# Kernel optimization log

Hardware: AMD Instinct MI355X
Metric: run time of the kernel (lower is better)

The kernel has to match this reference:

```python
import jax, jax.numpy as jnp
import numpy as np

IN_V, OUT_V, IN_E = 64, 64, 64
B, N, E = 2, 1024, 8192


def setup_inputs() -> dict:
    key = jax.random.key(0)
    ks = jax.random.split(key, 8)
    return {
        "H_v": jax.random.normal(ks[0], (B * N, IN_V), dtype=jnp.float32),
        "H_e": jax.random.normal(ks[1], (B * E, IN_E), dtype=jnp.float32),
        "adj_e": jax.random.uniform(ks[2], (B * E, E), dtype=jnp.float32),
        "adj_v": jax.random.uniform(ks[3], (B * N, N), dtype=jnp.float32),
        "T": jax.random.uniform(ks[4], (B * N, E), dtype=jnp.float32),
        "weight": jax.random.normal(ks[5], (IN_V, OUT_V), dtype=jnp.float32) * (1.0 / np.sqrt(OUT_V)),
        "p": jax.random.normal(ks[6], (1, IN_E), dtype=jnp.float32),
        "bias": jax.random.normal(ks[7], (OUT_V,), dtype=jnp.float32) * (1.0 / np.sqrt(OUT_V)),
    }


def reference(H_v, H_e, adj_e, adj_v, T, weight, p, bias):
    # node_layer=True branch of AlternateConvolution
    b = adj_v.shape[0] // adj_v.shape[1]
    n = adj_v.shape[1]
    e = adj_e.shape[1]
    H_v = H_v.reshape(b, n, -1)            # [B,N,in_v]
    H_e = H_e.reshape(b, e, -1)            # [B,E,in_e]
    adj_v = adj_v.reshape(b, n, n)         # [B,N,N]
    T = T.reshape(b, n, e)                 # [B,N,E]
    # diag_embed(H_e @ p^T) then T @ diag @ T^T == row-scale T by (H_e @ p^T) then GEMM
    scale = jnp.einsum('bef,f->be', H_e, p[0])                  # [B,E]
    multiplier1 = jnp.einsum('bne,be,bme->bnm', T, scale, T)    # [B,N,N]
    eye = jnp.eye(n, dtype=bool)
    M1 = jnp.where(eye[None, :, :], jnp.ones_like(multiplier1), multiplier1)
    adjusted_A = M1 * adj_v
    output = jnp.einsum('bnm,bmd->bnd', adjusted_A, H_v @ weight) + bias
    return output, H_e
```

## Files before the change

kernel.cpp:

```cpp
#include <hip/hip_runtime.h>

#define Bb 2
#define Nn 1024
#define Ee 8192
#define DV 64

typedef __attribute__((ext_vector_type(8))) short short8;
typedef __attribute__((ext_vector_type(4))) float floatx4;

static __device__ __forceinline__ unsigned short f2bf(float f) {
    unsigned int u = __float_as_uint(f);
    unsigned int r = (u + 0x7FFFu + ((u >> 16) & 1u)) >> 16;
    return (unsigned short)r;
}

__global__ __launch_bounds__(256) void scale_kernel(const float* __restrict__ He,
                                                    const float* __restrict__ p,
                                                    float* __restrict__ scale) {
    int wave = threadIdx.x >> 6;
    int lane = threadIdx.x & 63;
    int row = blockIdx.x * 4 + wave;
    float v = He[row * 64 + lane] * p[lane];
    #pragma unroll
    for (int off = 32; off > 0; off >>= 1) v += __shfl_xor(v, off);
    if (lane == 0) scale[row] = v;
}

__global__ __launch_bounds__(256) void cast_kernel(const float* __restrict__ T,
                                                   const float* __restrict__ scale,
                                                   unsigned short* __restrict__ Tsc,
                                                   unsigned short* __restrict__ Tpl) {
    size_t i4 = (size_t)blockIdx.x * 256 + threadIdx.x;
    size_t e0 = i4 * 4;
    int b = (int)(e0 >> 23);
    int e = (int)(e0 & 8191);
    floatx4 t = *(const floatx4*)&T[e0];
    floatx4 s = *(const floatx4*)&scale[(size_t)b * Ee + e];
    ushort4 sc, pl;
    sc.x = f2bf(t.x * s.x); sc.y = f2bf(t.y * s.y);
    sc.z = f2bf(t.z * s.z); sc.w = f2bf(t.w * s.w);
    pl.x = f2bf(t.x); pl.y = f2bf(t.y);
    pl.z = f2bf(t.z); pl.w = f2bf(t.w);
    *(ushort4*)&Tsc[e0] = sc;
    *(ushort4*)&Tpl[e0] = pl;
}

__global__ __launch_bounds__(256) void hw_kernel(const float* __restrict__ Hv,
                                                 const float* __restrict__ W,
                                                 float* __restrict__ HWo) {
    __shared__ float Ws[64 * 64];
    __shared__ float Hvs[4 * 64];
    int t = threadIdx.x;
    for (int i = t; i < 4096; i += 256) Ws[i] = W[i];
    int r0 = blockIdx.x * 4;
    Hvs[t] = Hv[(size_t)r0 * 64 + t];
    __syncthreads();
    int d = t & 63, rr = t >> 6;
    float acc = 0.f;
    #pragma unroll
    for (int c = 0; c < 64; ++c) acc += Hvs[rr * 64 + c] * Ws[c * 64 + d];
    HWo[(size_t)(r0 + rr) * 64 + d] = acc;
}

__global__ __launch_bounds__(256, 2) void mm_kernel(const unsigned short* __restrict__ Tsc,
                                                    const unsigned short* __restrict__ Tpl,
                                                    float* __restrict__ Ppart) {
    __shared__ __attribute__((aligned(16))) unsigned short As[128 * 64];
    __shared__ __attribute__((aligned(16))) unsigned short Bs[128 * 64];
    const int t = threadIdx.x;
    const int tile = blockIdx.x;
    const int b = blockIdx.y;
    const int s = blockIdx.z;

    int i = 0, rem = tile;
    while (rem >= 8 - i) { rem -= 8 - i; ++i; }
    const int j = i + rem;
    const int n0 = i * 128, m0 = j * 128;

    const int lane = t & 63;
    const int w = t >> 6;
    const int wr = w >> 1, wc = w & 1;
    const int quad = lane >> 4;
    const int l15 = lane & 15;
    const int l7 = l15 & 7;

    const int lr = lane >> 3;
    const int lc = (lane & 7) ^ lr;

    const int kc0 = (s * 128) / 7 * 64;
    const int kc1 = ((s + 1) * 128) / 7 * 64;

    const unsigned short* gA = Tsc + ((size_t)b * Nn + n0 + w * 32 + lr) * Ee + kc0 + lc * 8;
    const unsigned short* gB = Tpl + ((size_t)b * Nn + m0 + w * 32 + lr) * Ee + kc0 + lc * 8;
    unsigned short* lA = As + (w * 32) * 64 + lane * 8;
    unsigned short* lB = Bs + (w * 32) * 64 + lane * 8;

    floatx4 acc[4][4];
    #pragma unroll
    for (int a = 0; a < 4; ++a)
        #pragma unroll
        for (int c = 0; c < 4; ++c) acc[a][c] = (floatx4){0.f, 0.f, 0.f, 0.f};

    for (int k0 = kc0; k0 < kc1; k0 += 64) {
        #pragma unroll
        for (int u = 0; u < 4; ++u) {
            __builtin_amdgcn_global_load_lds(
                (const __attribute__((address_space(1))) unsigned int*)(gA + (size_t)u * 8 * Ee),
                (__attribute__((address_space(3))) unsigned int*)(lA + u * 8 * 64), 16, 0, 0);
            __builtin_amdgcn_global_load_lds(
                (const __attribute__((address_space(1))) unsigned int*)(gB + (size_t)u * 8 * Ee),
                (__attribute__((address_space(3))) unsigned int*)(lB + u * 8 * 64), 16, 0, 0);
        }
        gA += 64; gB += 64;
        __syncthreads();
        #pragma unroll
        for (int kk8 = 0; kk8 < 8; kk8 += 4) {
            short8 af[4], bf[4];
            #pragma unroll
            for (int a = 0; a < 4; ++a)
                af[a] = *(const short8*)&As[(wr * 64 + a * 16 + l15) * 64 + ((kk8 + quad) ^ l7) * 8];
            #pragma unroll
            for (int c = 0; c < 4; ++c)
                bf[c] = *(const short8*)&Bs[(wc * 64 + c * 16 + l15) * 64 + ((kk8 + quad) ^ l7) * 8];
            #pragma unroll
            for (int a = 0; a < 4; ++a)
                #pragma unroll
                for (int c = 0; c < 4; ++c)
                    acc[a][c] = __builtin_amdgcn_mfma_f32_16x16x32_bf16(af[a], bf[c], acc[a][c], 0, 0, 0);
        }
        __syncthreads();
    }

    float* P = Ppart + (((size_t)(b * 36 + tile)) * 7 + s) * 16384;
    #pragma unroll
    for (int a = 0; a < 4; ++a)
        #pragma unroll
        for (int c = 0; c < 4; ++c)
            #pragma unroll
            for (int v = 0; v < 4; ++v) {
                int r = wr * 64 + a * 16 + quad * 4 + v;
                int cc = wc * 64 + c * 16 + l15;
                P[r * 128 + cc] = acc[a][c][v];
            }
}

__global__ __launch_bounds__(256) void reduce_kernel(const float* __restrict__ Ppart,
                                                     const float* __restrict__ adj_v,
                                                     float* __restrict__ Aout) {
    __shared__ float Ls[64 * 133];
    const int t = threadIdx.x;
    const int job = blockIdx.x;
    const int h = blockIdx.y;
    const int b = job / 36;
    const int tile = job % 36;
    int i = 0, rem = tile;
    while (rem >= 8 - i) { rem -= 8 - i; ++i; }
    const int j = i + rem;
    const int n0 = i * 128, m0 = j * 128;
    const float* P = Ppart + (size_t)job * 7 * 16384;
    const float* AV = adj_v + (size_t)b * Nn * Nn;
    float* AO = Aout + (size_t)b * Nn * Nn;

    #pragma unroll
    for (int it = 0; it < 8; ++it) {
        int f = it * 256 + t;
        int r = f >> 5;
        int c = (f & 31) * 4;
        floatx4 v = (floatx4){0.f, 0.f, 0.f, 0.f};
        #pragma unroll
        for (int s = 0; s < 7; ++s) {
            floatx4 pv = *(const floatx4*)&P[s * 16384 + (h * 64 + r) * 128 + c];
            v.x += pv.x; v.y += pv.y; v.z += pv.z; v.w += pv.w;
        }
        int gn = n0 + h * 64 + r;
        int gm = m0 + c;
        if (i == j) {
            if (gn == gm) v.x = 1.f;
            if (gn == gm + 1) v.y = 1.f;
            if (gn == gm + 2) v.z = 1.f;
            if (gn == gm + 3) v.w = 1.f;
        }
        Ls[r * 133 + c] = v.x; Ls[r * 133 + c + 1] = v.y;
        Ls[r * 133 + c + 2] = v.z; Ls[r * 133 + c + 3] = v.w;
        floatx4 a = *(const floatx4*)&AV[(size_t)gn * Nn + gm];
        floatx4 o = (floatx4){v.x * a.x, v.y * a.y, v.z * a.z, v.w * a.w};
        *(floatx4*)&AO[(size_t)gn * Nn + gm] = o;
    }
    __syncthreads();
    if (i != j) {
        #pragma unroll
        for (int it = 0; it < 8; ++it) {
            int f = it * 256 + t;
            int m = f >> 4;
            int cn = (f & 15) * 4;
            floatx4 v;
            v.x = Ls[(cn + 0) * 133 + m];
            v.y = Ls[(cn + 1) * 133 + m];
            v.z = Ls[(cn + 2) * 133 + m];
            v.w = Ls[(cn + 3) * 133 + m];
            int grow = m0 + m;
            int gcol = n0 + h * 64 + cn;
            floatx4 a = *(const floatx4*)&AV[(size_t)grow * Nn + gcol];
            floatx4 o = (floatx4){v.x * a.x, v.y * a.y, v.z * a.z, v.w * a.w};
            *(floatx4*)&AO[(size_t)grow * Nn + gcol] = o;
        }
    }
}

__global__ __launch_bounds__(256) void out_kernel(const float* __restrict__ A,
                                                  const float* __restrict__ HWo,
                                                  const float* __restrict__ bias,
                                                  float* __restrict__ out) {
    __shared__ float HWs[64 * 64];
    __shared__ float Ash[8 * 64];
    int t = threadIdx.x;
    int b = blockIdx.y;
    int n0 = blockIdx.x * 8;
    int d = t & 63;
    int rr = t >> 6;
    float acc0 = 0.f, acc1 = 0.f;
    for (int m0 = 0; m0 < Nn; m0 += 64) {
        for (int i = t; i < 4096; i += 256) {
            int r = i >> 6, c = i & 63;
            HWs[i] = HWo[((size_t)b * Nn + m0 + r) * 64 + c];
        }
        {
            int i = t;
            int r = i >> 6, c = i & 63;
            Ash[i] = A[((size_t)b * Nn + n0 + r) * Nn + m0 + c];
            i += 256; r = i >> 6; c = i & 63;
            Ash[i] = A[((size_t)b * Nn + n0 + r) * Nn + m0 + c];
        }
        __syncthreads();
        #pragma unroll
        for (int mm = 0; mm < 64; ++mm) {
            float hw = HWs[mm * 64 + d];
            acc0 += Ash[rr * 64 + mm] * hw;
            acc1 += Ash[(rr + 4) * 64 + mm] * hw;
        }
        __syncthreads();
    }
    float bd = bias[d];
    out[((size_t)b * Nn + n0 + rr) * 64 + d] = acc0 + bd;
    out[((size_t)b * Nn + n0 + rr + 4) * 64 + d] = acc1 + bd;
}

extern "C" void kernel_launch(void* const* d_in, const int* in_sizes, int n_in,
                              void* d_out, int out_size, void* d_ws, size_t ws_size,
                              hipStream_t stream) {
    const float* H_v    = (const float*)d_in[0];
    const float* H_e    = (const float*)d_in[1];
    const float* adj_v  = (const float*)d_in[3];
    const float* T      = (const float*)d_in[4];
    const float* weight = (const float*)d_in[5];
    const float* p      = (const float*)d_in[6];
    const float* bias   = (const float*)d_in[7];
    float* out = (float*)d_out;

    char* ws = (char*)d_ws;
    float* scale          = (float*)ws;
    float* HWo            = (float*)(ws + (1 << 16));
    unsigned short* Tsc   = (unsigned short*)(ws + (1 << 20));
    unsigned short* Tpl   = (unsigned short*)(ws + (1 << 20) + (32u << 20));
    float* Ppart          = (float*)(ws + (1 << 20) + (64u << 20));
    float* Aout           = (float*)(ws + (1 << 20) + (98u << 20));

    hipMemcpyAsync(out + (size_t)Bb * Nn * DV, H_e,
                   (size_t)Bb * Ee * 64 * sizeof(float),
                   hipMemcpyDeviceToDevice, stream);

    scale_kernel<<<dim3(Bb * Ee / 4), dim3(256), 0, stream>>>(H_e, p, scale);
    cast_kernel<<<dim3((Bb * Nn * Ee / 4) / 256), dim3(256), 0, stream>>>(T, scale, Tsc, Tpl);
    hw_kernel<<<dim3(Bb * Nn / 4), dim3(256), 0, stream>>>(H_v, weight, HWo);
    mm_kernel<<<dim3(36, Bb, 7), dim3(256), 0, stream>>>(Tsc, Tpl, Ppart);
    reduce_kernel<<<dim3(36 * Bb, 2), dim3(256), 0, stream>>>(Ppart, adj_v, Aout);
    out_kernel<<<dim3(Nn / 8, Bb), dim3(256), 0, stream>>>(Aout, HWo, bias, out);
}
```

Baseline: 714.1 us.

## Fuse split-K reduce, adjacency masking and output GEMM with bf16 partials and atomics

```diff
diff --git a/kernel.cpp b/kernel.cpp
--- a/kernel.cpp
+++ b/kernel.cpp
@@ -6,12 +6,16 @@
 #define DV 64
 
 typedef __attribute__((ext_vector_type(8))) short short8;
+typedef __attribute__((ext_vector_type(8))) unsigned short ushort8;
 typedef __attribute__((ext_vector_type(4))) float floatx4;
 
 static __device__ __forceinline__ unsigned short f2bf(float f) {
     unsigned int u = __float_as_uint(f);
     unsigned int r = (u + 0x7FFFu + ((u >> 16) & 1u)) >> 16;
     return (unsigned short)r;
+}
+static __device__ __forceinline__ float bf2f(unsigned short u) {
+    return __uint_as_float(((unsigned int)u) << 16);
 }
 
 __global__ __launch_bounds__(256) void scale_kernel(const float* __restrict__ He,
@@ -62,9 +66,16 @@
     HWo[(size_t)(r0 + rr) * 64 + d] = acc;
 }
 
+__global__ __launch_bounds__(256) void binit_kernel(const float* __restrict__ bias,
+                                                    float* __restrict__ out) {
+    int idx = (blockIdx.x * 256 + threadIdx.x) * 4;
+    floatx4 bv = *(const floatx4*)&bias[idx & 63];
+    *(floatx4*)&out[idx] = bv;
+}
+
 __global__ __launch_bounds__(256, 2) void mm_kernel(const unsigned short* __restrict__ Tsc,
                                                     const unsigned short* __restrict__ Tpl,
-                                                    float* __restrict__ Ppart) {
+                                                    unsigned short* __restrict__ Ppart) {
     __shared__ __attribute__((aligned(16))) unsigned short As[128 * 64];
     __shared__ __attribute__((aligned(16))) unsigned short Bs[128 * 64];
     const int t = threadIdx.x;
@@ -131,7 +142,7 @@
         __syncthreads();
     }
 
-    float* P = Ppart + (((size_t)(b * 36 + tile)) * 7 + s) * 16384;
+    unsigned short* P = Ppart + (((size_t)(b * 36 + tile)) * 7 + s) * 16384;
     #pragma unroll
     for (int a = 0; a < 4; ++a)
         #pragma unroll
@@ -140,109 +151,134 @@
             for (int v = 0; v < 4; ++v) {
                 int r = wr * 64 + a * 16 + quad * 4 + v;
                 int cc = wc * 64 + c * 16 + l15;
-                P[r * 128 + cc] = acc[a][c][v];
+                P[r * 128 + cc] = f2bf(acc[a][c][v]);
             }
 }
 
-__global__ __launch_bounds__(256) void reduce_kernel(const float* __restrict__ Ppart,
-                                                     const float* __restrict__ adj_v,
-                                                     float* __restrict__ Aout) {
-    __shared__ float Ls[64 * 133];
+__global__ __launch_bounds__(256) void fuse_kernel(const unsigned short* __restrict__ Ppart,
+                                                   const float* __restrict__ adj_v,
+                                                   const float* __restrict__ HWo,
+                                                   float* __restrict__ out) {
+    __shared__ float Ls[64 * 68];
+    __shared__ float Lsn[64 * 68];
+    __shared__ float Lst[64 * 68];
     const int t = threadIdx.x;
     const int job = blockIdx.x;
-    const int h = blockIdx.y;
+    const int quad = blockIdx.y;
     const int b = job / 36;
     const int tile = job % 36;
     int i = 0, rem = tile;
     while (rem >= 8 - i) { rem -= 8 - i; ++i; }
     const int j = i + rem;
-    const int n0 = i * 128, m0 = j * 128;
-    const float* P = Ppart + (size_t)job * 7 * 16384;
+    const int qr = quad >> 1, qc = quad & 1;
+    const int n0 = i * 128 + qr * 64;
+    const int m0 = j * 128 + qc * 64;
+    const unsigned short* P = Ppart + (size_t)job * 7 * 16384 + (qr * 64) * 128 + qc * 64;
     const float* AV = adj_v + (size_t)b * Nn * Nn;
-    float* AO = Aout + (size_t)b * Nn * Nn;
-
-    #pragma unroll
-    for (int it = 0; it < 8; ++it) {
-        int f = it * 256 + t;
-        int r = f >> 5;
-        int c = (f & 31) * 4;
-        floatx4 v = (floatx4){0.f, 0.f, 0.f, 0.f};
-        #pragma unroll
-        for (int s = 0; s < 7; ++s) {
-            floatx4 pv = *(const floatx4*)&P[s * 16384 + (h * 64 + r) * 128 + c];
-            v.x += pv.x; v.y += pv.y; v.z += pv.z; v.w += pv.w;
-        }
-        int gn = n0 + h * 64 + r;
-        int gm = m0 + c;
-        if (i == j) {
-            if (gn == gm) v.x = 1.f;
-            if (gn == gm + 1) v.y = 1.f;
-            if (gn == gm + 2) v.z = 1.f;
-            if (gn == gm + 3) v.w = 1.f;
-        }
-        Ls[r * 133 + c] = v.x; Ls[r * 133 + c + 1] = v.y;
-        Ls[r * 133 + c + 2] = v.z; Ls[r * 133 + c + 3] = v.w;
-        floatx4 a = *(const floatx4*)&AV[(size_t)gn * Nn + gm];
-        floatx4 o = (floatx4){v.x * a.x, v.y * a.y, v.z * a.z, v.w * a.w};
-        *(floatx4*)&AO[(size_t)gn * Nn + gm] = o;
+    const float* HW = HWo + (size_t)b * Nn * 64;
+
+    {
+        int r = t >> 2, c0 = (t & 3) * 16;
+        float sv[16];
+        #pragma unroll
+        for (int x = 0; x < 16; ++x) sv[x] = 0.f;
+        #pragma unroll
+        for (int sp = 0; sp < 7; ++sp) {
+            const unsigned short* ps = P + sp * 16384 + r * 128 + c0;
+            ushort8 u0 = *(const ushort8*)ps;
+            ushort8 u1 = *(const ushort8*)(ps + 8);
+            #pragma unroll
+            for (int x = 0; x < 8; ++x) {
+                sv[x] += bf2f(u0[x]);
+                sv[8 + x] += bf2f(u1[x]);
+            }
+        }
+        if (i == j && qr == qc) {
+            int dcol = r - c0;
+            if (dcol >= 0 && dcol < 16) sv[dcol] = 1.0f;
+        }
+        #pragma unroll
+        for (int x4 = 0; x4 < 4; ++x4) {
+            floatx4 v = (floatx4){sv[x4 * 4], sv[x4 * 4 + 1], sv[x4 * 4 + 2], sv[x4 * 4 + 3]};
+            *(floatx4*)&Ls[r * 68 + c0 + x4 * 4] = v;
+            floatx4 a = *(const floatx4*)&AV[(size_t)(n0 + r) * Nn + m0 + c0 + x4 * 4];
+            floatx4 o = (floatx4){v.x * a.x, v.y * a.y, v.z * a.z, v.w * a.w};
+            *(floatx4*)&Lsn[r * 68 + c0 + x4 * 4] = o;
+        }
     }
     __syncthreads();
     if (i != j) {
-        #pragma unroll
-        for (int it = 0; it < 8; ++it) {
-            int f = it * 256 + t;
-            int m = f >> 4;
-            int cn = (f & 15) * 4;
-            floatx4 v;
-            v.x = Ls[(cn + 0) * 133 + m];
-            v.y = Ls[(cn + 1) * 133 + m];
-            v.z = Ls[(cn + 2) * 133 + m];
-            v.w = Ls[(cn + 3) * 133 + m];
-            int grow = m0 + m;
-            int gcol = n0 + h * 64 + cn;
-            floatx4 a = *(const floatx4*)&AV[(size_t)grow * Nn + gcol];
-            floatx4 o = (floatx4){v.x * a.x, v.y * a.y, v.z * a.z, v.w * a.w};
-            *(floatx4*)&AO[(size_t)grow * Nn + gcol] = o;
-        }
-    }
-}
-
-__global__ __launch_bounds__(256) void out_kernel(const float* __restrict__ A,
-                                                  const float* __restrict__ HWo,
-                                                  const float* __restrict__ bias,
-                                                  float* __restrict__ out) {
-    __shared__ float HWs[64 * 64];
-    __shared__ float Ash[8 * 64];
-    int t = threadIdx.x;
-    int b = blockIdx.y;
-    int n0 = blockIdx.x * 8;
-    int d = t & 63;
-    int rr = t >> 6;
-    float acc0 = 0.f, acc1 = 0.f;
-    for (int m0 = 0; m0 < Nn; m0 += 64) {
-        for (int i = t; i < 4096; i += 256) {
-            int r = i >> 6, c = i & 63;
-            HWs[i] = HWo[((size_t)b * Nn + m0 + r) * 64 + c];
-        }
-        {
-            int i = t;
-            int r = i >> 6, c = i & 63;
-            Ash[i] = A[((size_t)b * Nn + n0 + r) * Nn + m0 + c];
-            i += 256; r = i >> 6; c = i & 63;
-            Ash[i] = A[((size_t)b * Nn + n0 + r) * Nn + m0 + c];
-        }
-        __syncthreads();
-        #pragma unroll
-        for (int mm = 0; mm < 64; ++mm) {
-            float hw = HWs[mm * 64 + d];
-            acc0 += Ash[rr * 64 + mm] * hw;
-            acc1 += Ash[(rr + 4) * 64 + mm] * hw;
-        }
-        __syncthreads();
-    }
-    float bd = bias[d];
-    out[((size_t)b * Nn + n0 + rr) * 64 + d] = acc0 + bd;
-    out[((size_t)b * Nn + n0 + rr + 4) * 64 + d] = acc1 + bd;
+        int m = t >> 2, r0 = (t & 3) * 16;
+        #pragma unroll
+        for (int x4 = 0; x4 < 4; ++x4) {
+            floatx4 a = *(const floatx4*)&AV[(size_t)(m0 + m) * Nn + n0 + r0 + x4 * 4];
+            floatx4 o;
+            o.x = Ls[(r0 + x4 * 4 + 0) * 68 + m] * a.x;
+            o.y = Ls[(r0 + x4 * 4 + 1) * 68 + m] * a.y;
+            o.z = Ls[(r0 + x4 * 4 + 2) * 68 + m] * a.z;
+            o.w = Ls[(r0 + x4 * 4 + 3) * 68 + m] * a.w;
+            *(floatx4*)&Lst[m * 68 + r0 + x4 * 4] = o;
+        }
+    }
+    __syncthreads();
+
+    const int tr = t >> 4, tc = t & 15;
+    {
+        floatx4 acc[4];
+        #pragma unroll
+        for (int ii = 0; ii < 4; ++ii) acc[ii] = (floatx4){0.f, 0.f, 0.f, 0.f};
+        #pragma unroll
+        for (int k4 = 0; k4 < 64; k4 += 4) {
+            floatx4 bmat[4];
+            #pragma unroll
+            for (int u = 0; u < 4; ++u)
+                bmat[u] = *(const floatx4*)&HW[(size_t)(m0 + k4 + u) * 64 + tc * 4];
+            #pragma unroll
+            for (int ii = 0; ii < 4; ++ii) {
+                floatx4 av = *(const floatx4*)&Lsn[(tr * 4 + ii) * 68 + k4];
+                acc[ii] += av.x * bmat[0];
+                acc[ii] += av.y * bmat[1];
+                acc[ii] += av.z * bmat[2];
+                acc[ii] += av.w * bmat[3];
+            }
+        }
+        #pragma unroll
+        for (int ii = 0; ii < 4; ++ii) {
+            float* op = &out[(size_t)(b * Nn + n0 + tr * 4 + ii) * 64 + tc * 4];
+            atomicAdd(op + 0, acc[ii].x);
+            atomicAdd(op + 1, acc[ii].y);
+            atomicAdd(op + 2, acc[ii].z);
+            atomicAdd(op + 3, acc[ii].w);
+        }
+    }
+    if (i != j) {
+        floatx4 acc[4];
+        #pragma unroll
+        for (int ii = 0; ii < 4; ++ii) acc[ii] = (floatx4){0.f, 0.f, 0.f, 0.f};
+        #pragma unroll
+        for (int k4 = 0; k4 < 64; k4 += 4) {
+            floatx4 bmat[4];
+            #pragma unroll
+            for (int u = 0; u < 4; ++u)
+                bmat[u] = *(const floatx4*)&HW[(size_t)(n0 + k4 + u) * 64 + tc * 4];
+            #pragma unroll
+            for (int ii = 0; ii < 4; ++ii) {
+                floatx4 av = *(const floatx4*)&Lst[(tr * 4 + ii) * 68 + k4];
+                acc[ii] += av.x * bmat[0];
+                acc[ii] += av.y * bmat[1];
+                acc[ii] += av.z * bmat[2];
+                acc[ii] += av.w * bmat[3];
+            }
+        }
+        #pragma unroll
+        for (int ii = 0; ii < 4; ++ii) {
+            float* op = &out[(size_t)(b * Nn + m0 + tr * 4 + ii) * 64 + tc * 4];
+            atomicAdd(op + 0, acc[ii].x);
+            atomicAdd(op + 1, acc[ii].y);
+            atomicAdd(op + 2, acc[ii].z);
+            atomicAdd(op + 3, acc[ii].w);
+        }
+    }
 }
 
 extern "C" void kernel_launch(void* const* d_in, const int* in_sizes, int n_in,
@@ -262,17 +298,16 @@
     float* HWo            = (float*)(ws + (1 << 16));
     unsigned short* Tsc   = (unsigned short*)(ws + (1 << 20));
     unsigned short* Tpl   = (unsigned short*)(ws + (1 << 20) + (32u << 20));
-    float* Ppart          = (float*)(ws + (1 << 20) + (64u << 20));
-    float* Aout           = (float*)(ws + (1 << 20) + (98u << 20));
+    unsigned short* Ppart = (unsigned short*)(ws + (1 << 20) + (64u << 20));
 
     hipMemcpyAsync(out + (size_t)Bb * Nn * DV, H_e,
                    (size_t)Bb * Ee * 64 * sizeof(float),
                    hipMemcpyDeviceToDevice, stream);
 
+    binit_kernel<<<dim3((Bb * Nn * DV) / 1024), dim3(256), 0, stream>>>(bias, out);
     scale_kernel<<<dim3(Bb * Ee / 4), dim3(256), 0, stream>>>(H_e, p, scale);
     cast_kernel<<<dim3((Bb * Nn * Ee / 4) / 256), dim3(256), 0, stream>>>(T, scale, Tsc, Tpl);
     hw_kernel<<<dim3(Bb * Nn / 4), dim3(256), 0, stream>>>(H_v, weight, HWo);
     mm_kernel<<<dim3(36, Bb, 7), dim3(256), 0, stream>>>(Tsc, Tpl, Ppart);
-    reduce_kernel<<<dim3(36 * Bb, 2), dim3(256), 0, stream>>>(Ppart, adj_v, Aout);
-    out_kernel<<<dim3(Nn / 8, Bb), dim3(256), 0, stream>>>(Aout, HWo, bias, out);
-}
+    fuse_kernel<<<dim3(36 * Bb, 4), dim3(256), 0, stream>>>(Ppart, adj_v, HWo, out);
+}
```

After: 710.1 us. No clear change (-0.6%).
